# Kernel tuning notes

Measured on AMD Instinct MI355X. Metric: run time of the kernel, lower is better.

## Reference

```python
import jax, jax.numpy as jnp
import numpy as np

N, E, G = 20000, 320000, 64
DIN, H, EF, FC, OUT = 128, 256, 16, 256, 1
BN_EPS = 1e-5


def _gine_layer(x, src, dst, edge_attr, We, be, Wa, ba, g, bt, Wb, bb):
    # GINEConv (eps=0): out = mlp(x + sum_j relu(x_j + lin_edge(e_ij)))
    e = edge_attr @ We.T + be                      # [E, in_ch]
    m = jax.nn.relu(x[src] + e)                    # messages [E, in_ch]
    agg = jax.ops.segment_sum(m, dst, num_segments=x.shape[0])
    h = (x + agg) @ Wa.T + ba                      # Linear
    # BatchNorm1d in eval mode with running_mean=0, running_var=1
    inv = jax.lax.rsqrt(jnp.asarray(1.0 + BN_EPS, h.dtype))
    h = jax.nn.relu(h * inv * g + bt)
    return jax.nn.relu(h @ Wb.T + bb)


def _mean_pool(h, batch, num_graphs):
    sums = jax.ops.segment_sum(h, batch, num_segments=num_graphs)
    cnt = jax.ops.segment_sum(jnp.ones((h.shape[0],), h.dtype), batch, num_segments=num_graphs)
    return sums / jnp.maximum(cnt, 1.0)[:, None]


def setup_inputs() -> dict:
    key = jax.random.key(0)
    ks = iter(jax.random.split(key, 64))

    def nrm(shape, s=0.05):
        return jax.random.normal(next(ks), shape, jnp.float32) * s

    inp = {
        "x": jax.random.normal(next(ks), (N, DIN), jnp.float32),
        "edge_attr": jax.random.normal(next(ks), (E, EF), jnp.float32),
        "src": jax.random.randint(next(ks), (E,), 0, N),
        "dst": jax.random.randint(next(ks), (E,), 0, N),
        "batch": jnp.sort(jax.random.randint(next(ks), (N,), 0, G)),
    }
    dims = [(DIN, H), (H, H), (H, H)]
    for i, (din, h) in enumerate(dims, start=1):
        inp[f"We{i}"] = nrm((din, EF));  inp[f"be{i}"] = jnp.zeros((din,), jnp.float32)
        inp[f"Wa{i}"] = nrm((h, din));  inp[f"ba{i}"] = jnp.zeros((h,), jnp.float32)
        inp[f"g{i}"] = jnp.ones((h,), jnp.float32); inp[f"bt{i}"] = jnp.zeros((h,), jnp.float32)
        inp[f"Wb{i}"] = nrm((h, h));    inp[f"bb{i}"] = jnp.zeros((h,), jnp.float32)
    inp["L1w"] = nrm((FC * 3, H * 3)); inp["L1b"] = jnp.zeros((FC * 3,), jnp.float32)
    inp["L2w"] = nrm((OUT, FC * 3));   inp["L2b"] = jnp.zeros((OUT,), jnp.float32)
    return inp


def reference(x, edge_attr, src, dst, batch,
              We1, be1, Wa1, ba1, g1, bt1, Wb1, bb1,
              We2, be2, Wa2, ba2, g2, bt2, Wb2, bb2,
              We3, be3, Wa3, ba3, g3, bt3, Wb3, bb3,
              L1w, L1b, L2w, L2b):
    h1 = _gine_layer(x,  src, dst, edge_attr, We1, be1, Wa1, ba1, g1, bt1, Wb1, bb1)
    h2 = _gine_layer(h1, src, dst, edge_attr, We2, be2, Wa2, ba2, g2, bt2, Wb2, bb2)
    h3 = _gine_layer(h2, src, dst, edge_attr, We3, be3, Wa3, ba3, g3, bt3, Wb3, bb3)
    p = jnp.concatenate([_mean_pool(h1, batch, G),
                         _mean_pool(h2, batch, G),
                         _mean_pool(h3, batch, G)], axis=1)   # [G, 3H]
    h = jax.nn.relu(p @ L1w.T + L1b)   # dropout is identity (training=False)
    return jax.nn.sigmoid(h @ L2w.T + L2b)
```

## Files before the change

### kernel.cpp

```cpp
#include <hip/hip_runtime.h>
#include <math.h>
#include <stdint.h>

#define N_NODES 20000
#define M_PAD 20032
#define N_EDGES 320000
#define N_GRAPHS 64
#define DIN 128
#define H 256
#define POOL_W 768

typedef __attribute__((ext_vector_type(8))) short bf16x8;
typedef __attribute__((ext_vector_type(4))) float f32x4;
typedef __attribute__((ext_vector_type(4))) unsigned int u32x4;
typedef __attribute__((ext_vector_type(2))) unsigned int u32x2;
typedef _Float16 h2 __attribute__((ext_vector_type(2)));

__device__ __forceinline__ unsigned short f2bf(float f) {
    unsigned u = __builtin_bit_cast(unsigned, f);
    u += 0x7FFFu + ((u >> 16) & 1u);
    return (unsigned short)(u >> 16);
}
__device__ __forceinline__ float bf2f(unsigned short u) {
    return __builtin_bit_cast(float, (unsigned)u << 16);
}
__device__ __forceinline__ unsigned short f2h(float f) {
    const _Float16 h = (_Float16)f;
    return __builtin_bit_cast(unsigned short, h);
}

#if __has_builtin(__builtin_amdgcn_fdot2)
#define DOT2(a, b, c) __builtin_amdgcn_fdot2((a), (b), (c), false)
#else
__device__ __forceinline__ float dot2_fallback(h2 a, h2 b, float c) {
    return fmaf((float)a.x, (float)b.x, fmaf((float)a.y, (float)b.y, c));
}
#define DOT2(a, b, c) dot2_fallback((a), (b), (c))
#endif

struct CvtJob  { const float* s; unsigned short* d; int n4; int mode; };
struct CvtJobs { CvtJob j[12]; };

__global__ __launch_bounds__(256) void cvt_all(CvtJobs jobs)
{
    const CvtJob J = jobs.j[blockIdx.y];
    if (J.mode == 2) {
        const ushort4 z = {0, 0, 0, 0};
        for (int i = blockIdx.x * 256 + threadIdx.x; i < J.n4; i += gridDim.x * 256)
            ((ushort4*)J.d)[i] = z;
        return;
    }
    if (J.mode == 1) {
        for (int i = blockIdx.x * 256 + threadIdx.x; i < J.n4; i += gridDim.x * 256) {
            const float4 v = ((const float4*)J.s)[i];
            ushort4 r;
            r.x = f2h(v.x); r.y = f2h(v.y); r.z = f2h(v.z); r.w = f2h(v.w);
            ((ushort4*)J.d)[i] = r;
        }
        return;
    }
    for (int i = blockIdx.x * 256 + threadIdx.x; i < J.n4; i += gridDim.x * 256) {
        const float4 v = ((const float4*)J.s)[i];
        ushort4 r;
        r.x = f2bf(v.x); r.y = f2bf(v.y); r.z = f2bf(v.z); r.w = f2bf(v.w);
        ((ushort4*)J.d)[i] = r;
    }
}

__global__ __launch_bounds__(256) void hist_kernel(const int* __restrict__ dst,
                                                   int* __restrict__ deg)
{
    const int i = blockIdx.x * 256 + threadIdx.x;
    if (i < N_EDGES) atomicAdd(deg + dst[i], 1);
}

__global__ __launch_bounds__(1024) void scan_kernel(const int* __restrict__ deg,
                                                    int* __restrict__ off,
                                                    int* __restrict__ cur,
                                                    const int* __restrict__ batch,
                                                    int* __restrict__ start)
{
    __shared__ int wsum[16];
    __shared__ int carry;
    const int tid = threadIdx.x, wave = tid >> 6, lane = tid & 63;
    if (tid == 0) carry = 0;
    __syncthreads();
    for (int base = 0; base < N_NODES; base += 1024) {
        const int i = base + tid;
        const int v = (i < N_NODES) ? deg[i] : 0;
        int s = v;
#pragma unroll
        for (int d = 1; d < 64; d <<= 1) {
            const int t = __shfl_up(s, d);
            if (lane >= d) s += t;
        }
        if (lane == 63) wsum[wave] = s;
        __syncthreads();
        if (wave == 0) {
            int t = (lane < 16) ? wsum[lane] : 0;
#pragma unroll
            for (int d = 1; d < 16; d <<= 1) {
                const int u = __shfl_up(t, d);
                if (lane >= d) t += u;
            }
            if (lane < 16) wsum[lane] = t;
        }
        __syncthreads();
        const int wbase = (wave == 0) ? 0 : wsum[wave - 1];
        if (i < N_NODES) {
            const int o = carry + wbase + s - v;
            off[i] = o;
            cur[i] = o;
        }
        const int tot = wsum[15];
        __syncthreads();
        if (tid == 0) carry += tot;
        __syncthreads();
    }
    if (tid == 0) off[N_NODES] = carry;

    if (tid <= N_GRAPHS) {
        if (tid == N_GRAPHS) { start[N_GRAPHS] = N_NODES; }
        else {
            int lo = 0, hi = N_NODES;
            while (lo < hi) { const int mid = (lo + hi) >> 1; if (batch[mid] < tid) lo = mid + 1; else hi = mid; }
            start[tid] = lo;
        }
    }
}

__global__ __launch_bounds__(256) void scatter_kernel(
    const int* __restrict__ src, const int* __restrict__ dst,
    const float* __restrict__ ea, int* __restrict__ cursor,
    int* __restrict__ ssrc, unsigned short* __restrict__ eas)
{
    const int e = blockIdx.x * 256 + threadIdx.x;
    if (e < N_EDGES) {
        const int p = atomicAdd(cursor + dst[e], 1);
        ssrc[p] = src[e];
        const float4* er = (const float4*)(ea + (size_t)e * 16);
        unsigned short* dr = eas + (size_t)p * 16;
        ushort4* d4 = (ushort4*)dr;
#pragma unroll
        for (int q = 0; q < 4; ++q) {
            const float4 v = er[q];
            ushort4 r;
            r.x = f2h(v.x); r.y = f2h(v.y); r.z = f2h(v.z); r.w = f2h(v.w);
            d4[q] = r;
        }
    }
}

template<int IN>
__global__ __launch_bounds__(256, 4) void agg3(
    const unsigned short* __restrict__ xb,
    const unsigned short* __restrict__ eas,
    const int* __restrict__ ssrc,
    const int* __restrict__ off,
    const unsigned short* __restrict__ Weh,
    const float* __restrict__ be,
    unsigned short* __restrict__ out)
{
    constexpr int CPL = IN / 64;
    constexpr int XW  = CPL / 2;
    const int lane = threadIdx.x & 63;
    const int node = blockIdx.x * 4 + (threadIdx.x >> 6);
    if (node >= N_NODES) return;
    const int c0 = lane * CPL;
    const int zd = __builtin_amdgcn_mbcnt_lo(0u, 0u);

    u32x4 wlo[CPL], whi[CPL];
    float bias[CPL], acc[CPL];
#pragma unroll
    for (int j = 0; j < CPL; ++j) {
        const u32x4* wr = (const u32x4*)(Weh + (size_t)(c0 + j) * 16);
        wlo[j] = wr[0];
        whi[j] = wr[1];
        bias[j] = be[c0 + j];
        acc[j]  = 0.0f;
    }
#pragma unroll
    for (int j = 0; j < CPL; ++j) {
#pragma unroll
        for (int k = 0; k < 4; ++k) {
            { float t = __builtin_bit_cast(float, wlo[j][k]); asm volatile("" : "+v"(t)); wlo[j][k] = __builtin_bit_cast(unsigned int, t); }
            { float t = __builtin_bit_cast(float, whi[j][k]); asm volatile("" : "+v"(t)); whi[j][k] = __builtin_bit_cast(unsigned int, t); }
        }
        asm volatile("" : "+v"(bias[j]));
    }

    const int p0 = __builtin_amdgcn_readfirstlane(off[node]);
    const int p1 = __builtin_amdgcn_readfirstlane(off[node + 1]);
    const int n  = p1 - p0;

    auto ldsrc = [&](int i) -> int {
        const int q = (i < n) ? i : (n - 1);
        return ssrc[p0 + q + zd];
    };
    auto ldeL = [&](int i) -> u32x4 {
        const int q = (i < n) ? i : (n - 1);
        return ((const u32x4*)(eas + (size_t)(p0 + q + zd) * 16))[0];
    };
    auto ldeH = [&](int i) -> u32x4 {
        const int q = (i < n) ? i : (n - 1);
        return ((const u32x4*)(eas + (size_t)(p0 + q + zd) * 16))[1];
    };
    auto ldx = [&](int s) -> u32x2 {
        if constexpr (XW == 2) {
            return *(const u32x2*)(xb + (size_t)s * IN + c0);
        } else {
            u32x2 r;
            r[0] = *(const unsigned int*)(xb + (size_t)s * IN + c0);
            r[1] = 0u;
            return r;
        }
    };
    auto edge_compute = [&](u32x4 eL, u32x4 eH, u32x2 xw) {
        float m[CPL];
#pragma unroll
        for (int j = 0; j < CPL; ++j) m[j] = bias[j];
#pragma unroll
        for (int k = 0; k < 4; ++k) {
            const h2 ep = __builtin_bit_cast(h2, eL[k]);
#pragma unroll
            for (int j = 0; j < CPL; ++j)
                m[j] = DOT2(ep, __builtin_bit_cast(h2, wlo[j][k]), m[j]);
        }
#pragma unroll
        for (int k = 0; k < 4; ++k) {
            const h2 ep = __builtin_bit_cast(h2, eH[k]);
#pragma unroll
            for (int j = 0; j < CPL; ++j)
                m[j] = DOT2(ep, __builtin_bit_cast(h2, whi[j][k]), m[j]);
        }
#pragma unroll
        for (int j = 0; j < CPL; ++j) {
            const unsigned int word = xw[j >> 1];
            const float xf = __builtin_bit_cast(float,
                (j & 1) ? (word & 0xFFFF0000u) : (word << 16));
            acc[j] += fmaxf(m[j] + xf, 0.0f);
        }
    };

    if (n > 0) {
        int sA = ldsrc(0), sB = ldsrc(1), sC = ldsrc(2), sD = ldsrc(3);
        u32x4 eLA = ldeL(0), eHA = ldeH(0);
        u32x4 eLB = ldeL(1), eHB = ldeH(1);
        u32x4 eLC = ldeL(2), eHC = ldeH(2);
        u32x4 eLD = ldeL(3), eHD = ldeH(3);
        u32x2 xA = ldx(sA), xB = ldx(sB), xC = ldx(sC), xD = ldx(sD);
        sA = ldsrc(4); sB = ldsrc(5); sC = ldsrc(6); sD = ldsrc(7);

        int i = 0;
        for (; i + 4 <= n; i += 4) {
            edge_compute(eLA, eHA, xA);
            eLA = ldeL(i + 4); eHA = ldeH(i + 4); xA = ldx(sA); sA = ldsrc(i + 8);
            edge_compute(eLB, eHB, xB);
            eLB = ldeL(i + 5); eHB = ldeH(i + 5); xB = ldx(sB); sB = ldsrc(i + 9);
            edge_compute(eLC, eHC, xC);
            eLC = ldeL(i + 6); eHC = ldeH(i + 6); xC = ldx(sC); sC = ldsrc(i + 10);
            edge_compute(eLD, eHD, xD);
            eLD = ldeL(i + 7); eHD = ldeH(i + 7); xD = ldx(sD); sD = ldsrc(i + 11);
        }
        if (i < n)     edge_compute(eLA, eHA, xA);
        if (i + 1 < n) edge_compute(eLB, eHB, xB);
        if (i + 2 < n) edge_compute(eLC, eHC, xC);
    }

    if constexpr (XW == 2) {
        const u32x2 xs = *(const u32x2*)(xb + (size_t)node * IN + c0);
        const float x0 = __builtin_bit_cast(float, xs[0] << 16);
        const float x1 = __builtin_bit_cast(float, xs[0] & 0xFFFF0000u);
        const float x2 = __builtin_bit_cast(float, xs[1] << 16);
        const float x3 = __builtin_bit_cast(float, xs[1] & 0xFFFF0000u);
        u32x2 o;
        o[0] = (unsigned)f2bf(x0 + acc[0]) | ((unsigned)f2bf(x1 + acc[1]) << 16);
        o[1] = (unsigned)f2bf(x2 + acc[2]) | ((unsigned)f2bf(x3 + acc[3]) << 16);
        *(u32x2*)(out + (size_t)node * IN + c0) = o;
    } else {
        const unsigned int xs = *(const unsigned int*)(xb + (size_t)node * IN + c0);
        const float x0 = __builtin_bit_cast(float, xs << 16);
        const float x1 = __builtin_bit_cast(float, xs & 0xFFFF0000u);
        const unsigned int o =
            (unsigned)f2bf(x0 + acc[0]) | ((unsigned)f2bf(x1 + acc[1]) << 16);
        *(unsigned int*)(out + (size_t)node * IN + c0) = o;
    }
}

template<int K, int EPI>
__global__ __launch_bounds__(256) void gemm_breg2(
    const unsigned short* __restrict__ A,
    const unsigned short* __restrict__ W,
    const float* __restrict__ bias,
    const float* __restrict__ gsc, const float* __restrict__ bsh,
    unsigned short* __restrict__ out)
{
    constexpr int KC = K / 32;
    const int w = threadIdx.x >> 6, lane = threadIdx.x & 63;
    const int lm = lane & 15, lq = lane >> 4;
    const int n0 = (blockIdx.y * 4 + w) * 32;
    const int m0 = blockIdx.x * 64;

    bf16x8 B0[KC], B1[KC];
    {
        const unsigned short* Wp0 = W + (size_t)(n0 + lm) * K + lq * 8;
        const unsigned short* Wp1 = W + (size_t)(n0 + 16 + lm) * K + lq * 8;
#pragma unroll
        for (int c = 0; c < KC; ++c) {
            B0[c] = *(const bf16x8*)(Wp0 + c * 32);
            B1[c] = *(const bf16x8*)(Wp1 + c * 32);
        }
    }

    const float inv = rsqrtf(1.0f + 1e-5f);
    const float bc0 = bias[n0 + lm],      bc1 = bias[n0 + 16 + lm];
    const float gc0 = (EPI == 0) ? gsc[n0 + lm]      : 0.0f;
    const float gc1 = (EPI == 0) ? gsc[n0 + 16 + lm] : 0.0f;
    const float sc0 = (EPI == 0) ? bsh[n0 + lm]      : 0.0f;
    const float sc1 = (EPI == 0) ? bsh[n0 + 16 + lm] : 0.0f;

    bf16x8 aC[KC], aN[KC];
    {
        const unsigned short* Ap = A + (size_t)(m0 + lm) * K + lq * 8;
#pragma unroll
        for (int c = 0; c < KC; ++c) aC[c] = *(const bf16x8*)(Ap + c * 32);
    }

#pragma unroll
    for (int ch = 0; ch < 4; ++ch) {
        if (ch < 3) {
            const unsigned short* Ap = A + (size_t)(m0 + (ch + 1) * 16 + lm) * K + lq * 8;
#pragma unroll
            for (int c = 0; c < KC; ++c) aN[c] = *(const bf16x8*)(Ap + c * 32);
        }

        f32x4 acc0 = (f32x4){0.f, 0.f, 0.f, 0.f};
        f32x4 acc1 = (f32x4){0.f, 0.f, 0.f, 0.f};
#pragma unroll
        for (int c = 0; c < KC; ++c) {
            acc0 = __builtin_amdgcn_mfma_f32_16x16x32_bf16(aC[c], B0[c], acc0, 0, 0, 0);
            acc1 = __builtin_amdgcn_mfma_f32_16x16x32_bf16(aC[c], B1[c], acc1, 0, 0, 0);
        }

        const int mr = m0 + ch * 16;
#pragma unroll
        for (int r = 0; r < 4; ++r) {
            const int row = mr + lq * 4 + r;
            if (EPI == 1 && row >= N_NODES) continue;
            float v0 = acc0[r] + bc0;
            float v1 = acc1[r] + bc1;
            if (EPI == 0) {
                v0 = fmaxf(v0 * inv * gc0 + sc0, 0.0f);
                v1 = fmaxf(v1 * inv * gc1 + sc1, 0.0f);
            } else {
                v0 = fmaxf(v0, 0.0f);
                v1 = fmaxf(v1, 0.0f);
            }
            out[(size_t)row * H + n0 + lm]      = f2bf(v0);
            out[(size_t)row * H + n0 + 16 + lm] = f2bf(v1);
        }

#pragma unroll
        for (int c = 0; c < KC; ++c) aC[c] = aN[c];
    }
}

#define RSPLIT 6
__global__ __launch_bounds__(256) void pool2(
    const unsigned short* __restrict__ h1, const unsigned short* __restrict__ h2,
    const unsigned short* __restrict__ h3, const int* __restrict__ start,
    float* __restrict__ pool)
{
    const int g = blockIdx.x & 63, layer = blockIdx.x >> 6;
    const unsigned short* h = (layer == 0) ? h1 : (layer == 1) ? h2 : h3;
    const int r0 = start[g], r1 = start[g + 1];
    const int nr = r1 - r0;
    if (nr <= 0) return;
    const int chunk = (nr + RSPLIT - 1) / RSPLIT;
    const int rs = r0 + blockIdx.y * chunk;
    const int re = (rs + chunk < r1) ? rs + chunk : r1;
    if (rs >= re) return;

    const int c = threadIdx.x;
    float s0 = 0.f, s1 = 0.f, s2 = 0.f, s3 = 0.f;
    int r = rs;
    for (; r + 4 <= re; r += 4) {
        s0 += bf2f(h[(size_t)(r + 0) * H + c]);
        s1 += bf2f(h[(size_t)(r + 1) * H + c]);
        s2 += bf2f(h[(size_t)(r + 2) * H + c]);
        s3 += bf2f(h[(size_t)(r + 3) * H + c]);
    }
    for (; r < re; ++r) s0 += bf2f(h[(size_t)r * H + c]);
    atomicAdd(&pool[(size_t)g * POOL_W + layer * 256 + c], s0 + s1 + s2 + s3);
}

__global__ __launch_bounds__(256) void fc_head(
    const float* __restrict__ pool, const int* __restrict__ start,
    const float* __restrict__ L1w, const float* __restrict__ L1b,
    const float* __restrict__ L2w, float* __restrict__ gsum)
{
    const int g = blockIdx.x;
    __shared__ float p[POOL_W];

    const float rc = 1.0f / fmaxf((float)(start[g + 1] - start[g]), 1.0f);
    for (int i = threadIdx.x; i < POOL_W; i += 256)
        p[i] = pool[(size_t)g * POOL_W + i] * rc;
    __syncthreads();

    const int wv = threadIdx.x >> 6, lane = threadIdx.x & 63;
    const float4* p4 = (const float4*)p;
    const float4 pa = p4[lane], pb = p4[lane + 64], pc = p4[lane + 128];

    const int ob = blockIdx.y * 64 + wv * 16;
    float part = 0.0f;
#pragma unroll 4
    for (int t = 0; t < 16; ++t) {
        const int o = ob + t;
        const float4* wr = (const float4*)(L1w + (size_t)o * POOL_W);
        const float4 a = wr[lane], b = wr[lane + 64], c = wr[lane + 128];
        float acc = a.x * pa.x + a.y * pa.y + a.z * pa.z + a.w * pa.w
                  + b.x * pb.x + b.y * pb.y + b.z * pb.z + b.w * pb.w
                  + c.x * pc.x + c.y * pc.y + c.z * pc.z + c.w * pc.w;
#pragma unroll
        for (int off = 32; off > 0; off >>= 1) acc += __shfl_xor(acc, off);
        if (lane == 0) part += fmaxf(acc + L1b[o], 0.0f) * L2w[o];
    }
    if (lane == 0) atomicAdd(&gsum[g], part);
}

__global__ __launch_bounds__(64) void sig_kernel(
    const float* __restrict__ gsum, const float* __restrict__ L2b,
    float* __restrict__ out)
{
    const int g = threadIdx.x;
    if (g < N_GRAPHS) out[g] = 1.0f / (1.0f + expf(-(gsum[g] + L2b[0])));
}

extern "C" void kernel_launch(void* const* d_in, const int* in_sizes, int n_in,
                              void* d_out, int out_size, void* d_ws, size_t ws_size,
                              hipStream_t stream)
{
    const float* x     = (const float*)d_in[0];
    const float* ea    = (const float*)d_in[1];
    const int*   src   = (const int*)d_in[2];
    const int*   dst   = (const int*)d_in[3];
    const int*   batch = (const int*)d_in[4];

    const float* We[3]; const float* be[3]; const float* Wa[3]; const float* ba[3];
    const float* gg[3]; const float* bt[3]; const float* Wb[3]; const float* bb[3];
    for (int l = 0; l < 3; ++l) {
        const int o = 5 + 8 * l;
        We[l] = (const float*)d_in[o + 0]; be[l] = (const float*)d_in[o + 1];
        Wa[l] = (const float*)d_in[o + 2]; ba[l] = (const float*)d_in[o + 3];
        gg[l] = (const float*)d_in[o + 4]; bt[l] = (const float*)d_in[o + 5];
        Wb[l] = (const float*)d_in[o + 6]; bb[l] = (const float*)d_in[o + 7];
    }
    const float* L1w = (const float*)d_in[29];
    const float* L1b = (const float*)d_in[30];
    const float* L2w = (const float*)d_in[31];
    const float* L2b = (const float*)d_in[32];

    float* pool   = (float*)d_ws;
    float* gsum   = pool + (size_t)N_GRAPHS * POOL_W;
    int*   deg    = (int*)(gsum + N_GRAPHS);
    int*   off    = deg + N_NODES;
    int*   cursor = off + N_NODES + 1;
    int*   start  = cursor + N_NODES;
    int*   ssrc   = (int*)((((uintptr_t)(start + 72)) + 31) & ~(uintptr_t)31);
    unsigned short* eas = (unsigned short*)((((uintptr_t)(ssrc + N_EDGES)) + 31) & ~(uintptr_t)31);
    unsigned short* xb = (unsigned short*)((((uintptr_t)(eas + (size_t)N_EDGES * 16)) + 31) & ~(uintptr_t)31);
    unsigned short* u  = xb + (size_t)M_PAD * DIN;
    unsigned short* tT = u  + (size_t)M_PAD * H;
    unsigned short* h1 = tT + (size_t)M_PAD * H;
    unsigned short* h2 = h1 + (size_t)M_PAD * H;
    unsigned short* h3 = h2 + (size_t)M_PAD * H;
    unsigned short* wbf[6];
    wbf[0] = h3 + (size_t)M_PAD * H;
    wbf[1] = wbf[0] + H * DIN;
    for (int i = 2; i < 6; ++i) wbf[i] = wbf[i - 1] + H * H;
    unsigned short* weh[3];
    weh[0] = wbf[5] + H * H;
    weh[1] = weh[0] + DIN * 16;
    weh[2] = weh[1] + H * 16;

    CvtJobs jobs;
    jobs.j[0]  = { x,       xb,                    N_NODES * DIN / 4,       0 };
    jobs.j[1]  = { Wa[0],   wbf[0],                H * DIN / 4,             0 };
    jobs.j[2]  = { Wb[0],   wbf[1],                H * H / 4,               0 };
    jobs.j[3]  = { Wa[1],   wbf[2],                H * H / 4,               0 };
    jobs.j[4]  = { Wb[1],   wbf[3],                H * H / 4,               0 };
    jobs.j[5]  = { Wa[2],   wbf[4],                H * H / 4,               0 };
    jobs.j[6]  = { Wb[2],   wbf[5],                H * H / 4,               0 };
    jobs.j[7]  = { nullptr, (unsigned short*)deg,  N_NODES * 4 / 8,         2 };
    jobs.j[8]  = { nullptr, (unsigned short*)pool, (N_GRAPHS * POOL_W + N_GRAPHS) * 4 / 8, 2 };
    jobs.j[9]  = { We[0],   weh[0],                DIN * 16 / 4,            1 };
    jobs.j[10] = { We[1],   weh[1],                H * 16 / 4,              1 };
    jobs.j[11] = { We[2],   weh[2],                H * 16 / 4,              1 };
    cvt_all<<<dim3(320, 12), 256, 0, stream>>>(jobs);

    hist_kernel<<<(N_EDGES + 255) / 256, 256, 0, stream>>>(dst, deg);
    scan_kernel<<<1, 1024, 0, stream>>>(deg, off, cursor, batch, start);
    scatter_kernel<<<(N_EDGES + 255) / 256, 256, 0, stream>>>(src, dst, ea, cursor, ssrc, eas);

    const int  agrid = (N_NODES + 3) / 4;
    const dim3 ggrid(M_PAD / 64, 2);

    agg3<DIN><<<agrid, 256, 0, stream>>>(xb, eas, ssrc, off, weh[0], be[0], u);
    gemm_breg2<DIN, 0><<<ggrid, 256, 0, stream>>>(u, wbf[0], ba[0], gg[0], bt[0], tT);
    gemm_breg2<H,   1><<<ggrid, 256, 0, stream>>>(tT, wbf[1], bb[0], nullptr, nullptr, h1);
    agg3<H><<<agrid, 256, 0, stream>>>(h1, eas, ssrc, off, weh[1], be[1], u);
    gemm_breg2<H, 0><<<ggrid, 256, 0, stream>>>(u, wbf[2], ba[1], gg[1], bt[1], tT);
    gemm_breg2<H, 1><<<ggrid, 256, 0, stream>>>(tT, wbf[3], bb[1], nullptr, nullptr, h2);
    agg3<H><<<agrid, 256, 0, stream>>>(h2, eas, ssrc, off, weh[2], be[2], u);
    gemm_breg2<H, 0><<<ggrid, 256, 0, stream>>>(u, wbf[4], ba[2], gg[2], bt[2], tT);
    gemm_breg2<H, 1><<<ggrid, 256, 0, stream>>>(tT, wbf[5], bb[2], nullptr, nullptr, h3);

    pool2<<<dim3(3 * N_GRAPHS, RSPLIT), 256, 0, stream>>>(h1, h2, h3, start, pool);
    fc_head<<<dim3(N_GRAPHS, POOL_W / 64), 256, 0, stream>>>(pool, start, L1w, L1b, L2w, gsum);
    sig_kernel<<<1, 64, 0, stream>>>(gsum, L2b, (float*)d_out);
}
```

Baseline: 518.3 us.

## Balance edge aggregation by assigning fixed edge chunks to each wavefront

Replaces the one-wavefront-per-node aggregation with a merge-path style split: a new kernel binary-searches the CSR offsets to map each 40-edge chunk to a starting node, and each wavefront walks its node range, flushing accumulators at node boundaries. The aim is to even out work across wavefronts, avoid pipeline-prefetch waste on low-degree nodes, and keep the 4-deep load pipeline full across node boundaries. In exchange it adds a small extra kernel, per-edge boundary checks, and padding of the edge buffers for prefetch overrun. The occupancy hint on the launch bounds is also dropped.

```diff
diff --git a/kernel.cpp b/kernel.cpp
--- a/kernel.cpp
+++ b/kernel.cpp
@@ -9,6 +9,8 @@
 #define DIN 128
 #define H 256
 #define POOL_W 768
+#define CHUNK 40
+#define NCHUNK (N_EDGES / CHUNK)
 
 typedef __attribute__((ext_vector_type(8))) short bf16x8;
 typedef __attribute__((ext_vector_type(4))) float f32x4;
@@ -129,6 +131,18 @@
     }
 }
 
+__global__ __launch_bounds__(256) void chunkmap_kernel(const int* __restrict__ off,
+                                                       int* __restrict__ cmap)
+{
+    const int w = blockIdx.x * 256 + threadIdx.x;
+    if (w > NCHUNK) return;
+    if (w == NCHUNK) { cmap[w] = N_NODES; return; }
+    const int target = w * CHUNK;
+    int lo = 0, hi = N_NODES;
+    while (lo < hi) { const int mid = (lo + hi) >> 1; if (off[mid] < target) lo = mid + 1; else hi = mid; }
+    cmap[w] = lo;
+}
+
 __global__ __launch_bounds__(256) void scatter_kernel(
     const int* __restrict__ src, const int* __restrict__ dst,
     const float* __restrict__ ea, int* __restrict__ cursor,
@@ -152,11 +166,12 @@
 }
 
 template<int IN>
-__global__ __launch_bounds__(256, 4) void agg3(
+__global__ __launch_bounds__(256) void agg3(
     const unsigned short* __restrict__ xb,
     const unsigned short* __restrict__ eas,
     const int* __restrict__ ssrc,
     const int* __restrict__ off,
+    const int* __restrict__ cmap,
     const unsigned short* __restrict__ Weh,
     const float* __restrict__ be,
     unsigned short* __restrict__ out)
@@ -164,8 +179,7 @@
     constexpr int CPL = IN / 64;
     constexpr int XW  = CPL / 2;
     const int lane = threadIdx.x & 63;
-    const int node = blockIdx.x * 4 + (threadIdx.x >> 6);
-    if (node >= N_NODES) return;
+    const int wid  = blockIdx.x * 4 + (threadIdx.x >> 6);
     const int c0 = lane * CPL;
     const int zd = __builtin_amdgcn_mbcnt_lo(0u, 0u);
 
@@ -189,21 +203,51 @@
         asm volatile("" : "+v"(bias[j]));
     }
 
-    const int p0 = __builtin_amdgcn_readfirstlane(off[node]);
-    const int p1 = __builtin_amdgcn_readfirstlane(off[node + 1]);
-    const int n  = p1 - p0;
-
-    auto ldsrc = [&](int i) -> int {
-        const int q = (i < n) ? i : (n - 1);
-        return ssrc[p0 + q + zd];
-    };
-    auto ldeL = [&](int i) -> u32x4 {
-        const int q = (i < n) ? i : (n - 1);
-        return ((const u32x4*)(eas + (size_t)(p0 + q + zd) * 16))[0];
-    };
-    auto ldeH = [&](int i) -> u32x4 {
-        const int q = (i < n) ? i : (n - 1);
-        return ((const u32x4*)(eas + (size_t)(p0 + q + zd) * 16))[1];
+    int n          = __builtin_amdgcn_readfirstlane(cmap[wid]);
+    const int nend = __builtin_amdgcn_readfirstlane(cmap[wid + 1]);
+    if (n >= nend) return;
+    int p          = __builtin_amdgcn_readfirstlane(off[n]);
+    const int pend = __builtin_amdgcn_readfirstlane(off[nend]);
+
+    auto flush = [&](int nn) {
+        if constexpr (XW == 2) {
+            const u32x2 xs = *(const u32x2*)(xb + (size_t)nn * IN + c0);
+            const float x0 = __builtin_bit_cast(float, xs[0] << 16);
+            const float x1 = __builtin_bit_cast(float, xs[0] & 0xFFFF0000u);
+            const float x2 = __builtin_bit_cast(float, xs[1] << 16);
+            const float x3 = __builtin_bit_cast(float, xs[1] & 0xFFFF0000u);
+            u32x2 o;
+            o[0] = (unsigned)f2bf(x0 + acc[0]) | ((unsigned)f2bf(x1 + acc[1]) << 16);
+            o[1] = (unsigned)f2bf(x2 + acc[2]) | ((unsigned)f2bf(x3 + acc[3]) << 16);
+            *(u32x2*)(out + (size_t)nn * IN + c0) = o;
+        } else {
+            const unsigned int xs = *(const unsigned int*)(xb + (size_t)nn * IN + c0);
+            const float x0 = __builtin_bit_cast(float, xs << 16);
+            const float x1 = __builtin_bit_cast(float, xs & 0xFFFF0000u);
+            const unsigned int o =
+                (unsigned)f2bf(x0 + acc[0]) | ((unsigned)f2bf(x1 + acc[1]) << 16);
+            *(unsigned int*)(out + (size_t)nn * IN + c0) = o;
+        }
+#pragma unroll
+        for (int j = 0; j < CPL; ++j) acc[j] = 0.0f;
+    };
+
+    int p1 = __builtin_amdgcn_readfirstlane(off[n + 1]);
+    while (p1 == p) {
+        flush(n); ++n;
+        if (n >= nend) return;
+        p1 = __builtin_amdgcn_readfirstlane(off[n + 1]);
+    }
+
+    auto ldeL = [&](int q) -> u32x4 {
+        return ((const u32x4*)(eas + (size_t)(q + zd) * 16))[0];
+    };
+    auto ldeH = [&](int q) -> u32x4 {
+        return ((const u32x4*)(eas + (size_t)(q + zd) * 16))[1];
+    };
+    auto ldsrc = [&](int q) -> int {
+        const int qc = (q < N_EDGES) ? q : (N_EDGES - 1);
+        return ssrc[qc + zd];
     };
     auto ldx = [&](int s) -> u32x2 {
         if constexpr (XW == 2) {
@@ -241,50 +285,45 @@
             acc[j] += fmaxf(m[j] + xf, 0.0f);
         }
     };
-
-    if (n > 0) {
-        int sA = ldsrc(0), sB = ldsrc(1), sC = ldsrc(2), sD = ldsrc(3);
-        u32x4 eLA = ldeL(0), eHA = ldeH(0);
-        u32x4 eLB = ldeL(1), eHB = ldeH(1);
-        u32x4 eLC = ldeL(2), eHC = ldeH(2);
-        u32x4 eLD = ldeL(3), eHD = ldeH(3);
-        u32x2 xA = ldx(sA), xB = ldx(sB), xC = ldx(sC), xD = ldx(sD);
-        sA = ldsrc(4); sB = ldsrc(5); sC = ldsrc(6); sD = ldsrc(7);
-
-        int i = 0;
-        for (; i + 4 <= n; i += 4) {
-            edge_compute(eLA, eHA, xA);
-            eLA = ldeL(i + 4); eHA = ldeH(i + 4); xA = ldx(sA); sA = ldsrc(i + 8);
-            edge_compute(eLB, eHB, xB);
-            eLB = ldeL(i + 5); eHB = ldeH(i + 5); xB = ldx(sB); sB = ldsrc(i + 9);
-            edge_compute(eLC, eHC, xC);
-            eLC = ldeL(i + 6); eHC = ldeH(i + 6); xC = ldx(sC); sC = ldsrc(i + 10);
-            edge_compute(eLD, eHD, xD);
-            eLD = ldeL(i + 7); eHD = ldeH(i + 7); xD = ldx(sD); sD = ldsrc(i + 11);
-        }
-        if (i < n)     edge_compute(eLA, eHA, xA);
-        if (i + 1 < n) edge_compute(eLB, eHB, xB);
-        if (i + 2 < n) edge_compute(eLC, eHC, xC);
-    }
-
-    if constexpr (XW == 2) {
-        const u32x2 xs = *(const u32x2*)(xb + (size_t)node * IN + c0);
-        const float x0 = __builtin_bit_cast(float, xs[0] << 16);
-        const float x1 = __builtin_bit_cast(float, xs[0] & 0xFFFF0000u);
-        const float x2 = __builtin_bit_cast(float, xs[1] << 16);
-        const float x3 = __builtin_bit_cast(float, xs[1] & 0xFFFF0000u);
-        u32x2 o;
-        o[0] = (unsigned)f2bf(x0 + acc[0]) | ((unsigned)f2bf(x1 + acc[1]) << 16);
-        o[1] = (unsigned)f2bf(x2 + acc[2]) | ((unsigned)f2bf(x3 + acc[3]) << 16);
-        *(u32x2*)(out + (size_t)node * IN + c0) = o;
-    } else {
-        const unsigned int xs = *(const unsigned int*)(xb + (size_t)node * IN + c0);
-        const float x0 = __builtin_bit_cast(float, xs << 16);
-        const float x1 = __builtin_bit_cast(float, xs & 0xFFFF0000u);
-        const unsigned int o =
-            (unsigned)f2bf(x0 + acc[0]) | ((unsigned)f2bf(x1 + acc[1]) << 16);
-        *(unsigned int*)(out + (size_t)node * IN + c0) = o;
-    }
+    auto adv = [&]() {
+        flush(n); ++n;
+        while (n < nend) {
+            p1 = __builtin_amdgcn_readfirstlane(off[n + 1]);
+            if (p1 != p) break;
+            flush(n); ++n;
+        }
+    };
+
+    int sA = ldsrc(p),     sB = ldsrc(p + 1), sC = ldsrc(p + 2), sD = ldsrc(p + 3);
+    u32x4 eLA = ldeL(p),     eHA = ldeH(p);
+    u32x4 eLB = ldeL(p + 1), eHB = ldeH(p + 1);
+    u32x4 eLC = ldeL(p + 2), eHC = ldeH(p + 2);
+    u32x4 eLD = ldeL(p + 3), eHD = ldeH(p + 3);
+    u32x2 xA = ldx(sA), xB = ldx(sB), xC = ldx(sC), xD = ldx(sD);
+    sA = ldsrc(p + 4); sB = ldsrc(p + 5); sC = ldsrc(p + 6); sD = ldsrc(p + 7);
+
+    for (;;) {
+        edge_compute(eLA, eHA, xA);
+        eLA = ldeL(p + 4); eHA = ldeH(p + 4); xA = ldx(sA); sA = ldsrc(p + 8);
+        ++p; if (p == p1) adv();
+        if (p >= pend) break;
+
+        edge_compute(eLB, eHB, xB);
+        eLB = ldeL(p + 4); eHB = ldeH(p + 4); xB = ldx(sB); sB = ldsrc(p + 8);
+        ++p; if (p == p1) adv();
+        if (p >= pend) break;
+
+        edge_compute(eLC, eHC, xC);
+        eLC = ldeL(p + 4); eHC = ldeH(p + 4); xC = ldx(sC); sC = ldsrc(p + 8);
+        ++p; if (p == p1) adv();
+        if (p >= pend) break;
+
+        edge_compute(eLD, eHD, xD);
+        eLD = ldeL(p + 4); eHD = ldeH(p + 4); xD = ldx(sD); sD = ldsrc(p + 8);
+        ++p; if (p == p1) adv();
+        if (p >= pend) break;
+    }
+    while (n < nend) { flush(n); ++n; }
 }
 
 template<int K, int EPI>
@@ -466,9 +505,10 @@
     int*   off    = deg + N_NODES;
     int*   cursor = off + N_NODES + 1;
     int*   start  = cursor + N_NODES;
-    int*   ssrc   = (int*)((((uintptr_t)(start + 72)) + 31) & ~(uintptr_t)31);
-    unsigned short* eas = (unsigned short*)((((uintptr_t)(ssrc + N_EDGES)) + 31) & ~(uintptr_t)31);
-    unsigned short* xb = (unsigned short*)((((uintptr_t)(eas + (size_t)N_EDGES * 16)) + 31) & ~(uintptr_t)31);
+    int*   cmap   = start + 72;
+    int*   ssrc   = (int*)((((uintptr_t)(cmap + NCHUNK + 1)) + 31) & ~(uintptr_t)31);
+    unsigned short* eas = (unsigned short*)((((uintptr_t)(ssrc + N_EDGES + 16)) + 31) & ~(uintptr_t)31);
+    unsigned short* xb = (unsigned short*)((((uintptr_t)(eas + (size_t)(N_EDGES + 16) * 16)) + 31) & ~(uintptr_t)31);
     unsigned short* u  = xb + (size_t)M_PAD * DIN;
     unsigned short* tT = u  + (size_t)M_PAD * H;
     unsigned short* h1 = tT + (size_t)M_PAD * H;
@@ -500,18 +540,19 @@
 
     hist_kernel<<<(N_EDGES + 255) / 256, 256, 0, stream>>>(dst, deg);
     scan_kernel<<<1, 1024, 0, stream>>>(deg, off, cursor, batch, start);
+    chunkmap_kernel<<<(NCHUNK + 256) / 256, 256, 0, stream>>>(off, cmap);
     scatter_kernel<<<(N_EDGES + 255) / 256, 256, 0, stream>>>(src, dst, ea, cursor, ssrc, eas);
 
-    const int  agrid = (N_NODES + 3) / 4;
+    const int  agrid = NCHUNK / 4;
     const dim3 ggrid(M_PAD / 64, 2);
 
-    agg3<DIN><<<agrid, 256, 0, stream>>>(xb, eas, ssrc, off, weh[0], be[0], u);
+    agg3<DIN><<<agrid, 256, 0, stream>>>(xb, eas, ssrc, off, cmap, weh[0], be[0], u);
     gemm_breg2<DIN, 0><<<ggrid, 256, 0, stream>>>(u, wbf[0], ba[0], gg[0], bt[0], tT);
     gemm_breg2<H,   1><<<ggrid, 256, 0, stream>>>(tT, wbf[1], bb[0], nullptr, nullptr, h1);
-    agg3<H><<<agrid, 256, 0, stream>>>(h1, eas, ssrc, off, weh[1], be[1], u);
+    agg3<H><<<agrid, 256, 0, stream>>>(h1, eas, ssrc, off, cmap, weh[1], be[1], u);
     gemm_breg2<H, 0><<<ggrid, 256, 0, stream>>>(u, wbf[2], ba[1], gg[1], bt[1], tT);
     gemm_breg2<H, 1><<<ggrid, 256, 0, stream>>>(tT, wbf[3], bb[1], nullptr, nullptr, h2);
-    agg3<H><<<agrid, 256, 0, stream>>>(h2, eas, ssrc, off, weh[2], be[2], u);
+    agg3<H><<<agrid, 256, 0, stream>>>(h2, eas, ssrc, off, cmap, weh[2], be[2], u);
     gemm_breg2<H, 0><<<ggrid, 256, 0, stream>>>(u, wbf[4], ba[2], gg[2], bt[2], tT);
     gemm_breg2<H, 1><<<ggrid, 256, 0, stream>>>(tT, wbf[5], bb[2], nullptr, nullptr, h3);
 
```

Measured after the change: 521.9 us. No clear change (+0.7%).
